# Performance work log

Hardware: AMD Instinct MI355X
Metric: run time of the kernel (lower is better)

Reference implementation:

```python
import jax, jax.numpy as jnp
import numpy as np

N = 16384      # total atoms (8 proteins x ~2048)
E = 524288     # N * max_neighbors(32)
B = 8          # graphs
F_IN = 26      # 20 residue types + 6 atom types
D = 128        # node_dim
H = 256        # hidden_dim
OUT = 64       # output_dim
L = 4          # n_layers
N_RBF = 16
CUTOFF = 10.0


def setup_inputs() -> dict:
    key = jax.random.key(0)
    ks = jax.random.split(key, 24)
    s = 0.05
    inp = {
        "positions": jax.random.normal(ks[0], (N, 3), jnp.float32) * 10.0,
        "node_features": jax.random.normal(ks[1], (N, F_IN), jnp.float32),
        "edge_index": jax.random.randint(ks[2], (2, E), 0, N, jnp.int32),
        "batch": jnp.sort(jax.random.randint(ks[3], (N,), 0, B, jnp.int32)),
        # node embedding MLP
        "emb_W1": jax.random.normal(ks[4], (F_IN, D), jnp.float32) * s,
        "emb_b1": jnp.zeros((D,), jnp.float32),
        "emb_W2": jax.random.normal(ks[5], (D, D), jnp.float32) * s,
        "emb_b2": jnp.zeros((D,), jnp.float32),
        # per-layer message MLP: [2D + n_rbf] -> H -> D
        "msg_W1": jax.random.normal(ks[6], (L, 2 * D + N_RBF, H), jnp.float32) * s,
        "msg_b1": jnp.zeros((L, H), jnp.float32),
        "msg_W2": jax.random.normal(ks[7], (L, H, D), jnp.float32) * s,
        "msg_b2": jnp.zeros((L, D), jnp.float32),
        # per-layer update MLP: [2D] -> H -> D (residual)
        "upd_W1": jax.random.normal(ks[8], (L, 2 * D, H), jnp.float32) * s,
        "upd_b1": jnp.zeros((L, H), jnp.float32),
        "upd_W2": jax.random.normal(ks[9], (L, H, D), jnp.float32) * s,
        "upd_b2": jnp.zeros((L, D), jnp.float32),
        # readout MLP: D -> H -> OUT
        "r_W1": jax.random.normal(ks[10], (D, H), jnp.float32) * s,
        "r_b1": jnp.zeros((H,), jnp.float32),
        "r_W2": jax.random.normal(ks[11], (H, OUT), jnp.float32) * s,
        "r_b2": jnp.zeros((OUT,), jnp.float32),
    }
    return inp


def _mlp2(x, W1, b1, W2, b2):
    return jax.nn.silu(x @ W1 + b1) @ W2 + b2


def _edge_rbf(positions, src, dst):
    rel = positions[dst] - positions[src]                      # (E,3)
    d = jnp.sqrt(jnp.sum(rel * rel, axis=-1) + 1e-12)          # (E,)
    centers = jnp.linspace(0.0, CUTOFF, N_RBF, dtype=positions.dtype)
    width = CUTOFF / N_RBF
    rbf = jnp.exp(-((d[:, None] - centers) ** 2) / (2.0 * width * width))  # (E,n_rbf)
    env = 0.5 * (jnp.cos(jnp.pi * d / CUTOFF) + 1.0) * (d < CUTOFF)        # cosine cutoff
    return rbf * env[:, None]


def reference(positions, node_features, edge_index, batch,
              emb_W1, emb_b1, emb_W2, emb_b2,
              msg_W1, msg_b1, msg_W2, msg_b2,
              upd_W1, upd_b1, upd_W2, upd_b2,
              r_W1, r_b1, r_W2, r_b2):
    src, dst = edge_index[0], edge_index[1]
    h = _mlp2(node_features, emb_W1, emb_b1, emb_W2, emb_b2)   # (N,D)
    ef = _edge_rbf(positions, src, dst)                        # (E,n_rbf)
    for i in range(L):
        m_in = jnp.concatenate([h[src], h[dst], ef], axis=-1)  # (E,2D+n_rbf)
        m = _mlp2(m_in, msg_W1[i], msg_b1[i], msg_W2[i], msg_b2[i])  # (E,D)
        agg = jax.ops.segment_sum(m, dst, num_segments=N)      # (N,D)
        u_in = jnp.concatenate([h, agg], axis=-1)              # (N,2D)
        h = h + _mlp2(u_in, upd_W1[i], upd_b1[i], upd_W2[i], upd_b2[i])
    # mean readout per graph
    counts = jax.ops.segment_sum(jnp.ones((N,), h.dtype), batch, num_segments=B)
    g = jax.ops.segment_sum(h, batch, num_segments=B) / jnp.maximum(counts, 1.0)[:, None]
    return _mlp2(g, r_W1, r_b1, r_W2, r_b2)                    # (B,OUT)
```

## Files before the change

### kernel.cpp

```cpp
#include <hip/hip_runtime.h>
#include <math.h>

#define NATOMS 16384
#define NEDGES 524288
#define NLAYERS 4
#define TE 64

typedef __bf16 bf16x8 __attribute__((ext_vector_type(8)));
typedef __bf16 bf16x4 __attribute__((ext_vector_type(4)));
typedef __bf16 bf16x2 __attribute__((ext_vector_type(2)));
typedef float f32x4 __attribute__((ext_vector_type(4)));

__device__ __forceinline__ float silu_f(float x) {
  return x * __builtin_amdgcn_rcpf(1.0f + __expf(-x));
}

__global__ __launch_bounds__(256) void hist_kernel(
    const int* __restrict__ dst, int* __restrict__ counts)
{
  int e = blockIdx.x * 256 + threadIdx.x;
  atomicAdd(&counts[dst[e]], 1);
}

__global__ __launch_bounds__(1024) void scan_kernel(
    const int* __restrict__ counts, int* __restrict__ cursor,
    float* __restrict__ degf)
{
  __shared__ int s_tot[1024];
  int tid = threadIdx.x;
  int v[16];
  {
    const int4* cp = (const int4*)(counts + tid * 16);
    int4 a = cp[0], b = cp[1], c = cp[2], d = cp[3];
    v[0]=a.x; v[1]=a.y; v[2]=a.z; v[3]=a.w;
    v[4]=b.x; v[5]=b.y; v[6]=b.z; v[7]=b.w;
    v[8]=c.x; v[9]=c.y; v[10]=c.z; v[11]=c.w;
    v[12]=d.x; v[13]=d.y; v[14]=d.z; v[15]=d.w;
  }
  int tot = 0;
  #pragma unroll
  for (int i = 0; i < 16; i++) tot += v[i];
  s_tot[tid] = tot;
  __syncthreads();
  for (int off = 1; off < 1024; off <<= 1) {
    int t = (tid >= off) ? s_tot[tid - off] : 0;
    __syncthreads();
    s_tot[tid] += t;
    __syncthreads();
  }
  int run = s_tot[tid] - tot;
  #pragma unroll
  for (int i = 0; i < 16; i++) {
    cursor[tid * 16 + i] = run;
    degf[tid * 16 + i] = (float)v[i];
    run += v[i];
  }
}

__global__ __launch_bounds__(256) void scatter_kernel(
    const int* __restrict__ src, const int* __restrict__ dst,
    int* __restrict__ cursor, int* __restrict__ esrc, int* __restrict__ edst)
{
  int e = blockIdx.x * 256 + threadIdx.x;
  int d = dst[e];
  int p = atomicAdd(&cursor[d], 1);
  esrc[p] = src[e];
  edst[p] = d;
}

__global__ __launch_bounds__(256) void prep_kernel(
    const float* __restrict__ mW1, const float* __restrict__ mW2,
    const float* __restrict__ uW1, const float* __restrict__ uW2,
    const float* __restrict__ mb2,
    __bf16* __restrict__ W1at, __bf16* __restrict__ W1bt,
    __bf16* __restrict__ B2c, __bf16* __restrict__ uW1ft,
    __bf16* __restrict__ uW2t, float* __restrict__ b2u)
{
  long l = blockIdx.y;
  int bx = blockIdx.x, tid = threadIdx.x;
  if (bx < 128) {
    int i = bx * 256 + tid;
    int n = i >> 7, k = i & 127;
    W1at[l * (256L * 128) + i] = (__bf16)mW1[l * (272L * 256) + (size_t)k * 256 + n];
  } else if (bx < 256) {
    int i = (bx - 128) * 256 + tid;
    int n = i >> 7, k = i & 127;
    W1bt[l * (256L * 128) + i] = (__bf16)mW1[l * (272L * 256) + (size_t)(128 + k) * 256 + n];
  } else if (bx < 288) {
    int i = (bx - 256) * 256 + tid;
    int c = i >> 5, k = i & 31;
    float v = (k < 16) ? mW1[l * (272L * 256) + (size_t)(256 + k) * 256 + c] : 0.0f;
    B2c[l * (256L * 32) + i] = (__bf16)v;
  } else if (bx < 672) {
    int i = (bx - 288) * 256 + tid;
    int n = i / 384, k = i - n * 384;
    float v;
    if (k < 128) {
      v = uW1[l * 65536 + (size_t)k * 256 + n];
    } else {
      int r = k - 128;
      v = 0.0f;
      for (int j = 0; j < 128; j++)
        v += mW2[(l * 256 + r) * 128 + j] * uW1[l * 65536 + (size_t)(128 + j) * 256 + n];
    }
    uW1ft[l * (256L * 384) + i] = (__bf16)v;
  } else if (bx < 800) {
    int i = (bx - 672) * 256 + tid;
    int n = i >> 8, k = i & 255;
    uW2t[l * (128L * 256) + i] = (__bf16)uW2[l * (256L * 128) + (size_t)k * 128 + n];
  } else {
    int c = tid;
    float acc = 0.0f;
    for (int j = 0; j < 128; j++)
      acc += mb2[l * 128 + j] * uW1[l * 65536 + (size_t)(128 + j) * 256 + c];
    b2u[l * 256 + c] = acc;
  }
}

__global__ __launch_bounds__(128) void embed_kernel(
    const float* __restrict__ x, const float* __restrict__ W1,
    const float* __restrict__ b1, const float* __restrict__ W2,
    const float* __restrict__ b2, float* __restrict__ h,
    __bf16* __restrict__ hb)
{
  int n = blockIdx.x;
  int j = threadIdx.x;
  __shared__ float xs[26];
  __shared__ float hid[128];
  if (j < 26) xs[j] = x[n * 26 + j];
  __syncthreads();
  float acc = b1[j];
  #pragma unroll
  for (int k = 0; k < 26; k++) acc += xs[k] * W1[k * 128 + j];
  hid[j] = silu_f(acc);
  __syncthreads();
  float acc2 = b2[j];
  #pragma unroll 8
  for (int k = 0; k < 128; k++) acc2 += hid[k] * W2[k * 128 + j];
  h[(size_t)n * 128 + j] = acc2;
  hb[(size_t)n * 128 + j] = (__bf16)acc2;
}

__global__ __launch_bounds__(256) void rbf_kernel(
    const float* __restrict__ pos, const int* __restrict__ esrc,
    const int* __restrict__ edst, __bf16* __restrict__ efb)
{
  int e = blockIdx.x * 256 + threadIdx.x;
  int s = esrc[e], d = edst[e];
  float dx = pos[d * 3 + 0] - pos[s * 3 + 0];
  float dy = pos[d * 3 + 1] - pos[s * 3 + 1];
  float dz = pos[d * 3 + 2] - pos[s * 3 + 2];
  float dist = sqrtf(dx * dx + dy * dy + dz * dz + 1e-12f);
  float env = (dist < 10.0f)
                  ? 0.5f * (cosf(3.14159265358979f * dist * 0.1f) + 1.0f)
                  : 0.0f;
  bf16x8 o0, o1;
  #pragma unroll
  for (int i = 0; i < 16; i++) {
    float c = (10.0f / 15.0f) * (float)i;
    float t = dist - c;
    float v = env * __expf(-t * t * 1.28f);
    if (i < 8) o0[i] = (__bf16)v; else o1[i - 8] = (__bf16)v;
  }
  *(bf16x8*)(efb + (size_t)e * 16 + 0) = o0;
  *(bf16x8*)(efb + (size_t)e * 16 + 8) = o1;
}

__global__ __launch_bounds__(256) void zprep_kernel(
    const __bf16* __restrict__ hb, const float* __restrict__ b1,
    const __bf16* __restrict__ W1at, const __bf16* __restrict__ W1bt,
    __bf16* __restrict__ z1b, __bf16* __restrict__ z2b, float* __restrict__ aggH)
{
  __shared__ __bf16 s_n[64][136];
  int tid = threadIdx.x, n0 = blockIdx.x * 64;
  {
    int n = tid >> 2, t4 = tid & 3;
    const bf16x8* hr = (const bf16x8*)(hb + (size_t)(n0 + n) * 128);
    #pragma unroll
    for (int i = 0; i < 4; i++)
      *(bf16x8*)&s_n[n][t4 * 8 + 32 * i] = hr[t4 + 4 * i];
  }
  {
    float4 zz = make_float4(0.f, 0.f, 0.f, 0.f);
    float4* ap = (float4*)(aggH + (size_t)n0 * 256);
    for (int i = tid; i < 64 * 256 / 4; i += 256) ap[i] = zz;
  }
  __syncthreads();
  const int wv = tid >> 6, ln = tid & 63, lc = ln & 15, qd = ln >> 4;
  for (int cp = 0; cp < 2; cp++) {
    f32x4 aA[4][2], aB[4][2];
    #pragma unroll
    for (int nt = 0; nt < 2; nt++) {
      float bv = b1[cp * 128 + wv * 32 + nt * 16 + lc];
      #pragma unroll
      for (int mt = 0; mt < 4; mt++) {
        aA[mt][nt][0] = 0.f; aA[mt][nt][1] = 0.f;
        aA[mt][nt][2] = 0.f; aA[mt][nt][3] = 0.f;
        aB[mt][nt][0] = bv; aB[mt][nt][1] = bv;
        aB[mt][nt][2] = bv; aB[mt][nt][3] = bv;
      }
    }
    #pragma unroll
    for (int kt = 0; kt < 4; kt++) {
      bf16x8 af[4];
      #pragma unroll
      for (int mt = 0; mt < 4; mt++)
        af[mt] = *(const bf16x8*)&s_n[mt * 16 + lc][kt * 32 + qd * 8];
      bf16x8 bwA[2], bwB[2];
      #pragma unroll
      for (int nt = 0; nt < 2; nt++) {
        int c = cp * 128 + wv * 32 + nt * 16 + lc;
        bwA[nt] = *(const bf16x8*)(W1at + (size_t)c * 128 + kt * 32 + qd * 8);
        bwB[nt] = *(const bf16x8*)(W1bt + (size_t)c * 128 + kt * 32 + qd * 8);
      }
      #pragma unroll
      for (int mt = 0; mt < 4; mt++)
        #pragma unroll
        for (int nt = 0; nt < 2; nt++) {
          aA[mt][nt] = __builtin_amdgcn_mfma_f32_16x16x32_bf16(af[mt], bwA[nt], aA[mt][nt], 0, 0, 0);
          aB[mt][nt] = __builtin_amdgcn_mfma_f32_16x16x32_bf16(af[mt], bwB[nt], aB[mt][nt], 0, 0, 0);
        }
    }
    #pragma unroll
    for (int mt = 0; mt < 4; mt++)
      #pragma unroll
      for (int nt = 0; nt < 2; nt++) {
        int c = cp * 128 + wv * 32 + nt * 16 + lc;
        #pragma unroll
        for (int r = 0; r < 4; r++) {
          int n = n0 + mt * 16 + qd * 4 + r;
          z1b[(size_t)n * 256 + c] = (__bf16)aA[mt][nt][r];
          z2b[(size_t)n * 256 + c] = (__bf16)aB[mt][nt][r];
        }
      }
  }
}

#define MS_EF_OFF   33792
#define MS_SRC_OFF  36864
#define MS_DST_OFF  37120
#define MS_MASK_OFF 37376
#define MS_BYTES    37392

__global__ __launch_bounds__(256, 4) void msg_mfma_kernel(
    const __bf16* __restrict__ z1b, const __bf16* __restrict__ z2b,
    const __bf16* __restrict__ efb,
    const int* __restrict__ esrc, const int* __restrict__ edst,
    const __bf16* __restrict__ B2c, float* __restrict__ aggH)
{
  __shared__ __align__(16) char smem[MS_BYTES];
  __bf16 (*s_hT)[66] = (__bf16(*)[66])(smem);
  __bf16 (*s_ef)[24] = (__bf16(*)[24])(smem + MS_EF_OFF);
  int* s_src = (int*)(smem + MS_SRC_OFF);
  int* s_dst = (int*)(smem + MS_DST_OFF);
  unsigned int* s_mask = (unsigned int*)(smem + MS_MASK_OFF);

  int tid = threadIdx.x, e0 = blockIdx.x * TE;

  if (tid < TE) {
    int d = edst[e0 + tid];
    s_dst[tid] = d;
    int dp = (tid == 0) ? (d ^ 1) : edst[e0 + tid - 1];
    unsigned long long mb = __ballot(d != dp);
    if (tid == 0) { s_mask[0] = (unsigned int)mb; s_mask[1] = (unsigned int)(mb >> 32); }
  } else if (tid < 2 * TE) {
    s_src[tid - TE] = esrc[e0 + tid - TE];
  }
  {
    int e = tid >> 2, t4 = tid & 3;
    if (t4 < 2)
      *(bf16x8*)&s_ef[e][t4 * 8] =
          *(const bf16x8*)(efb + (size_t)(e0 + e) * 16 + t4 * 8);
  }
  __syncthreads();

  const int wv = tid >> 6, ln = tid & 63, lc = ln & 15, qd = ln >> 4;

  bf16x8 bI;
  #pragma unroll
  for (int j = 0; j < 8; j++)
    bI[j] = (__bf16)((lc == (qd & 1) * 8 + j) ? 1.0f : 0.0f);

  const __bf16* pz[4];
  #pragma unroll
  for (int mt = 0; mt < 4; mt++) {
    int m = mt * 16 + lc;
    int row = (qd < 2) ? s_src[m] : s_dst[m];
    pz[mt] = ((qd < 2) ? z1b : z2b) + (size_t)row * 256 + (qd & 1) * 8;
  }

  #pragma unroll
  for (int hf = 0; hf < 2; hf++) {
    const int cb = hf * 128 + wv * 32;
    bf16x8 bw[2];
    #pragma unroll
    for (int nt = 0; nt < 2; nt++)
      bw[nt] = *(const bf16x8*)(B2c + (size_t)(cb + nt * 16 + lc) * 32 + qd * 8);

    #pragma unroll
    for (int mt = 0; mt < 4; mt++) {
      bf16x8 aef = *(const bf16x8*)&s_ef[mt * 16 + lc][(qd & 1) * 8];
      #pragma unroll
      for (int nt = 0; nt < 2; nt++) {
        bf16x8 az = *(const bf16x8*)(pz[mt] + cb + nt * 16);
        f32x4 z; z[0] = 0.f; z[1] = 0.f; z[2] = 0.f; z[3] = 0.f;
        f32x4 acc = __builtin_amdgcn_mfma_f32_16x16x32_bf16(az, bI, z, 0, 0, 0);
        acc = __builtin_amdgcn_mfma_f32_16x16x32_bf16(aef, bw[nt], acc, 0, 0, 0);
        bf16x2 p0, p1;
        p0[0] = (__bf16)silu_f(acc[0]); p0[1] = (__bf16)silu_f(acc[1]);
        p1[0] = (__bf16)silu_f(acc[2]); p1[1] = (__bf16)silu_f(acc[3]);
        __bf16* wp = &s_hT[cb + nt * 16 + lc][mt * 16 + qd * 4];
        *(bf16x2*)wp = p0;
        *(bf16x2*)(wp + 2) = p1;
      }
    }
  }
  __syncthreads();

  {
    const unsigned int mlo = __builtin_amdgcn_readfirstlane(s_mask[0]);
    const unsigned int mhi = __builtin_amdgcn_readfirstlane(s_mask[1]);
    int j = tid;
    float acc = 0.0f;
    int cur = s_dst[0];
    #pragma unroll 8
    for (int i = 0; i < 64; i += 2) {
      bf16x2 p = *(const bf16x2*)&s_hT[j][i];
      bool b0 = (i < 32) ? ((mlo >> i) & 1u) : ((mhi >> (i - 32)) & 1u);
      int i1 = i + 1;
      bool b1 = (i1 < 32) ? ((mlo >> i1) & 1u) : ((mhi >> (i1 - 32)) & 1u);
      if (i > 0 && b0) {
        atomicAdd(&aggH[(size_t)cur * 256 + j], acc);
        acc = 0.0f; cur = s_dst[i];
      }
      acc += (float)p[0];
      if (b1) {
        atomicAdd(&aggH[(size_t)cur * 256 + j], acc);
        acc = 0.0f; cur = s_dst[i1];
      }
      acc += (float)p[1];
    }
    atomicAdd(&aggH[(size_t)cur * 256 + j], acc);
  }
}

__global__ __launch_bounds__(512, 2) void upd_mfma_kernel(
    float* __restrict__ h, __bf16* __restrict__ hb,
    float* __restrict__ aggH, const float* __restrict__ degf,
    const __bf16* __restrict__ uW1ft, const float* __restrict__ b1,
    const float* __restrict__ b2u,
    const __bf16* __restrict__ uW2t, const float* __restrict__ b2,
    int do_z, const float* __restrict__ nb1,
    const __bf16* __restrict__ nW1at, const __bf16* __restrict__ nW1bt,
    __bf16* __restrict__ z1b, __bf16* __restrict__ z2b)
{
  __shared__ __bf16 s_u[64][392];
  __shared__ __bf16 s_uh[64][264];
  int tid = threadIdx.x, n0 = blockIdx.x * 64;
  {
    int n = tid >> 3, t8 = tid & 7;
    const bf16x8* hr = (const bf16x8*)(hb + (size_t)(n0 + n) * 128);
    #pragma unroll
    for (int i = 0; i < 2; i++)
      *(bf16x8*)&s_u[n][t8 * 8 + 64 * i] = hr[t8 + 8 * i];
    const float* sr = aggH + (size_t)(n0 + n) * 256;
    #pragma unroll
    for (int i = 0; i < 4; i++) {
      int col = t8 * 8 + i * 64;
      float4 a = *(const float4*)(sr + col);
      float4 b = *(const float4*)(sr + col + 4);
      bf16x8 o;
      o[0] = (__bf16)a.x; o[1] = (__bf16)a.y; o[2] = (__bf16)a.z; o[3] = (__bf16)a.w;
      o[4] = (__bf16)b.x; o[5] = (__bf16)b.y; o[6] = (__bf16)b.z; o[7] = (__bf16)b.w;
      *(bf16x8*)&s_u[n][128 + col] = o;
    }
  }
  __syncthreads();
  const int wv = tid >> 6, ln = tid & 63, lc = ln & 15, qd = ln >> 4;

  float dg[4][4];
  #pragma unroll
  for (int mt = 0; mt < 4; mt++)
    #pragma unroll
    for (int r = 0; r < 4; r++)
      dg[mt][r] = degf[n0 + mt * 16 + qd * 4 + r];

  {
    f32x4 acc1[4][2];
    #pragma unroll
    for (int nt = 0; nt < 2; nt++) {
      int c = wv * 32 + nt * 16 + lc;
      float bv = b1[c];
      float b2uv = b2u[c];
      #pragma unroll
      for (int mt = 0; mt < 4; mt++)
        #pragma unroll
        for (int r = 0; r < 4; r++)
          acc1[mt][nt][r] = bv + dg[mt][r] * b2uv;
    }
    #pragma unroll
    for (int kt = 0; kt < 12; kt++) {
      bf16x8 af[4];
      #pragma unroll
      for (int mt = 0; mt < 4; mt++)
        af[mt] = *(const bf16x8*)&s_u[mt * 16 + lc][kt * 32 + qd * 8];
      bf16x8 bw[2];
      #pragma unroll
      for (int nt = 0; nt < 2; nt++)
        bw[nt] = *(const bf16x8*)(uW1ft +
                 (size_t)(wv * 32 + nt * 16 + lc) * 384 + kt * 32 + qd * 8);
      #pragma unroll
      for (int mt = 0; mt < 4; mt++)
        #pragma unroll
        for (int nt = 0; nt < 2; nt++)
          acc1[mt][nt] = __builtin_amdgcn_mfma_f32_16x16x32_bf16(af[mt], bw[nt], acc1[mt][nt], 0, 0, 0);
    }
    #pragma unroll
    for (int mt = 0; mt < 4; mt++)
      #pragma unroll
      for (int nt = 0; nt < 2; nt++) {
        int cc = wv * 32 + nt * 16 + lc;
        #pragma unroll
        for (int r = 0; r < 4; r++)
          s_uh[mt * 16 + qd * 4 + r][cc] = (__bf16)silu_f(acc1[mt][nt][r]);
      }
  }
  __syncthreads();

  const int ow = wv * 16 + lc;
  f32x4 acc2[4];
  {
    float bv = b2[ow];
    #pragma unroll
    for (int mt = 0; mt < 4; mt++) {
      acc2[mt][0] = bv; acc2[mt][1] = bv; acc2[mt][2] = bv; acc2[mt][3] = bv;
    }
  }
  #pragma unroll
  for (int kt = 0; kt < 8; kt++) {
    bf16x8 a2[4];
    #pragma unroll
    for (int mt = 0; mt < 4; mt++)
      a2[mt] = *(const bf16x8*)&s_uh[mt * 16 + lc][kt * 32 + qd * 8];
    bf16x8 b2w = *(const bf16x8*)(uW2t + (size_t)ow * 256 + kt * 32 + qd * 8);
    #pragma unroll
    for (int mt = 0; mt < 4; mt++)
      acc2[mt] = __builtin_amdgcn_mfma_f32_16x16x32_bf16(a2[mt], b2w, acc2[mt], 0, 0, 0);
  }

  #pragma unroll
  for (int mt = 0; mt < 4; mt++)
    #pragma unroll
    for (int r = 0; r < 4; r++) {
      int n = n0 + mt * 16 + qd * 4 + r;
      float v = h[(size_t)n * 128 + ow] + acc2[mt][r];
      h[(size_t)n * 128 + ow] = v;
      hb[(size_t)n * 128 + ow] = (__bf16)v;
    }

  if (do_z) {
    __syncthreads();
    {
      float4 zz = make_float4(0.f, 0.f, 0.f, 0.f);
      float4* ap = (float4*)(aggH + (size_t)n0 * 256);
      for (int i = tid; i < 64 * 256 / 4; i += 512) ap[i] = zz;
      int n = tid >> 3, t8 = tid & 7;
      const bf16x8* hr = (const bf16x8*)(hb + (size_t)(n0 + n) * 128);
      #pragma unroll
      for (int i = 0; i < 2; i++)
        *(bf16x8*)&s_u[n][t8 * 8 + 64 * i] = hr[t8 + 8 * i];
    }
    __syncthreads();
    f32x4 aA[4][2], aB[4][2];
    #pragma unroll
    for (int nt = 0; nt < 2; nt++) {
      float bv = nb1[wv * 32 + nt * 16 + lc];
      #pragma unroll
      for (int mt = 0; mt < 4; mt++) {
        aA[mt][nt][0] = 0.f; aA[mt][nt][1] = 0.f;
        aA[mt][nt][2] = 0.f; aA[mt][nt][3] = 0.f;
        aB[mt][nt][0] = bv; aB[mt][nt][1] = bv;
        aB[mt][nt][2] = bv; aB[mt][nt][3] = bv;
      }
    }
    #pragma unroll
    for (int kt = 0; kt < 4; kt++) {
      bf16x8 af[4];
      #pragma unroll
      for (int mt = 0; mt < 4; mt++)
        af[mt] = *(const bf16x8*)&s_u[mt * 16 + lc][kt * 32 + qd * 8];
      bf16x8 bwA[2], bwB[2];
      #pragma unroll
      for (int nt = 0; nt < 2; nt++) {
        int c = wv * 32 + nt * 16 + lc;
        bwA[nt] = *(const bf16x8*)(nW1at + (size_t)c * 128 + kt * 32 + qd * 8);
        bwB[nt] = *(const bf16x8*)(nW1bt + (size_t)c * 128 + kt * 32 + qd * 8);
      }
      #pragma unroll
      for (int mt = 0; mt < 4; mt++)
        #pragma unroll
        for (int nt = 0; nt < 2; nt++) {
          aA[mt][nt] = __builtin_amdgcn_mfma_f32_16x16x32_bf16(af[mt], bwA[nt], aA[mt][nt], 0, 0, 0);
          aB[mt][nt] = __builtin_amdgcn_mfma_f32_16x16x32_bf16(af[mt], bwB[nt], aB[mt][nt], 0, 0, 0);
        }
    }
    #pragma unroll
    for (int mt = 0; mt < 4; mt++)
      #pragma unroll
      for (int nt = 0; nt < 2; nt++) {
        int c = wv * 32 + nt * 16 + lc;
        #pragma unroll
        for (int r = 0; r < 4; r++) {
          int n = n0 + mt * 16 + qd * 4 + r;
          z1b[(size_t)n * 256 + c] = (__bf16)aA[mt][nt][r];
          z2b[(size_t)n * 256 + c] = (__bf16)aB[mt][nt][r];
        }
      }
  }
}

__global__ __launch_bounds__(128) void readout_sum_kernel(
    const float* __restrict__ h, const int* __restrict__ batch,
    float* __restrict__ gsum, float* __restrict__ gcnt)
{
  int j = threadIdx.x;
  int n0 = blockIdx.x * 128;
  float acc = 0.f, cacc = 0.f;
  int cur = batch[n0];
  for (int i = 0; i < 128; i++) {
    int b = batch[n0 + i];
    if (b != cur) {
      atomicAdd(&gsum[cur * 128 + j], acc);
      if (j == 0) atomicAdd(&gcnt[cur], cacc);
      acc = 0.f; cacc = 0.f; cur = b;
    }
    acc += h[(size_t)(n0 + i) * 128 + j];
    cacc += 1.f;
  }
  atomicAdd(&gsum[cur * 128 + j], acc);
  if (j == 0) atomicAdd(&gcnt[cur], cacc);
}

__global__ __launch_bounds__(256) void readout_mlp_kernel(
    const float* __restrict__ gsum, const float* __restrict__ gcnt,
    const float* __restrict__ W1, const float* __restrict__ b1,
    const float* __restrict__ W2, const float* __restrict__ b2,
    float* __restrict__ out)
{
  __shared__ float g[8][128];
  __shared__ float hid[8][256];
  int tid = threadIdx.x;
  for (int i = tid; i < 8 * 128; i += 256) {
    int b = i >> 7, c = i & 127;
    g[b][c] = gsum[i] / fmaxf(gcnt[b], 1.0f);
  }
  __syncthreads();
  {
    float bb = b1[tid];
    float a[8];
    #pragma unroll
    for (int b = 0; b < 8; b++) a[b] = bb;
    for (int k = 0; k < 128; k++) {
      float w = W1[k * 256 + tid];
      #pragma unroll
      for (int b = 0; b < 8; b++) a[b] += g[b][k] * w;
    }
    #pragma unroll
    for (int b = 0; b < 8; b++) hid[b][tid] = silu_f(a[b]);
  }
  __syncthreads();
  int j = tid & 63, bg = tid >> 6;
  float a0 = b2[j], a1 = b2[j];
  for (int k = 0; k < 256; k++) {
    float w = W2[k * 64 + j];
    a0 += hid[bg * 2 + 0][k] * w;
    a1 += hid[bg * 2 + 1][k] * w;
  }
  out[(bg * 2 + 0) * 64 + j] = a0;
  out[(bg * 2 + 1) * 64 + j] = a1;
}

extern "C" void kernel_launch(void* const* d_in, const int* in_sizes, int n_in,
                              void* d_out, int out_size, void* d_ws, size_t ws_size,
                              hipStream_t stream) {
  const float* pos   = (const float*)d_in[0];
  const float* xfeat = (const float*)d_in[1];
  const int*   eidx  = (const int*)d_in[2];
  const int*   batch = (const int*)d_in[3];
  const float* eW1 = (const float*)d_in[4];
  const float* eb1 = (const float*)d_in[5];
  const float* eW2 = (const float*)d_in[6];
  const float* eb2 = (const float*)d_in[7];
  const float* mW1 = (const float*)d_in[8];
  const float* mb1 = (const float*)d_in[9];
  const float* mW2 = (const float*)d_in[10];
  const float* mb2 = (const float*)d_in[11];
  const float* uW1 = (const float*)d_in[12];
  const float* ub1 = (const float*)d_in[13];
  const float* uW2 = (const float*)d_in[14];
  const float* ub2 = (const float*)d_in[15];
  const float* rW1 = (const float*)d_in[16];
  const float* rb1 = (const float*)d_in[17];
  const float* rW2 = (const float*)d_in[18];
  const float* rb2 = (const float*)d_in[19];

  const int* srcI = eidx;
  const int* dstI = eidx + NEDGES;

  char* base = (char*)d_ws;
  float* h    = (float*)base;  base += (size_t)NATOMS * 128 * 4;
  float* aggH = (float*)base;  base += (size_t)NATOMS * 256 * 4;
  __bf16* z1b = (__bf16*)base; base += (size_t)NATOMS * 256 * 2;
  __bf16* z2b = (__bf16*)base; base += (size_t)NATOMS * 256 * 2;
  __bf16* hb  = (__bf16*)base; base += (size_t)NATOMS * 128 * 2;
  __bf16* efb = (__bf16*)base; base += (size_t)NEDGES * 16 * 2;
  __bf16* W1at = (__bf16*)base; base += (size_t)NLAYERS * 256 * 128 * 2;
  __bf16* W1bt = (__bf16*)base; base += (size_t)NLAYERS * 256 * 128 * 2;
  __bf16* B2c  = (__bf16*)base; base += (size_t)NLAYERS * 256 * 32 * 2;
  __bf16* uW1ft = (__bf16*)base; base += (size_t)NLAYERS * 256 * 384 * 2;
  __bf16* uW2t = (__bf16*)base; base += (size_t)NLAYERS * 128 * 256 * 2;
  float* b2u  = (float*)base;  base += (size_t)NLAYERS * 256 * 4;
  float* degf = (float*)base;  base += (size_t)NATOMS * 4;
  float* gsum = (float*)base;  base += 8 * 128 * 4;
  float* gcnt = (float*)base;  base += 8 * 4;
  int* counts = (int*)base;    base += (size_t)NATOMS * 4;
  int* cursor = (int*)base;    base += (size_t)NATOMS * 4;
  int* esrc   = (int*)base;    base += (size_t)NEDGES * 4;
  int* edst   = (int*)base;    base += (size_t)NEDGES * 4;

  hipMemsetAsync(counts, 0, NATOMS * sizeof(int), stream);
  hist_kernel<<<NEDGES / 256, 256, 0, stream>>>(dstI, counts);
  scan_kernel<<<1, 1024, 0, stream>>>(counts, cursor, degf);
  scatter_kernel<<<NEDGES / 256, 256, 0, stream>>>(srcI, dstI, cursor, esrc, edst);

  prep_kernel<<<dim3(801, NLAYERS), 256, 0, stream>>>(
      mW1, mW2, uW1, uW2, mb2, W1at, W1bt, B2c, uW1ft, uW2t, b2u);

  embed_kernel<<<NATOMS, 128, 0, stream>>>(xfeat, eW1, eb1, eW2, eb2, h, hb);
  rbf_kernel<<<NEDGES / 256, 256, 0, stream>>>(pos, esrc, edst, efb);

  zprep_kernel<<<NATOMS / 64, 256, 0, stream>>>(
      hb, mb1, W1at, W1bt, z1b, z2b, aggH);

  for (int l = 0; l < NLAYERS; l++) {
    int ln = (l < NLAYERS - 1) ? (l + 1) : l;
    msg_mfma_kernel<<<NEDGES / TE, 256, 0, stream>>>(
        z1b, z2b, efb, esrc, edst,
        B2c + (size_t)l * 256 * 32, aggH);
    upd_mfma_kernel<<<NATOMS / 64, 512, 0, stream>>>(
        h, hb, aggH, degf,
        uW1ft + (size_t)l * 256 * 384, ub1 + (size_t)l * 256,
        b2u + (size_t)l * 256,
        uW2t + (size_t)l * 128 * 256, ub2 + (size_t)l * 128,
        (l < NLAYERS - 1) ? 1 : 0,
        mb1 + (size_t)ln * 256,
        W1at + (size_t)ln * 256 * 128, W1bt + (size_t)ln * 256 * 128,
        z1b, z2b);
  }

  hipMemsetAsync(gsum, 0, (8 * 128 + 8) * sizeof(float), stream);
  readout_sum_kernel<<<NATOMS / 128, 128, 0, stream>>>(h, batch, gsum, gcnt);
  readout_mlp_kernel<<<1, 256, 0, stream>>>(gsum, gcnt, rW1, rb1, rW2, rb2,
                                            (float*)d_out);
}
```

Measured before the change: 674.9 us.

## Fuse embedding MLP into zprep and enlarge message edge tile to 128

The node embedding MLP is folded into the zprep kernel, so h is computed per 64-node tile and fed straight into shared memory, which removes one launch and a global round trip of hb. The message kernel now handles 128 edges per block with 512 threads: each wave covers one 32-column slice across 8 row tiles, and the segmented-sum reduction is split into two 64-edge halves with per-wave ballot masks. This halves the number of message blocks and gives more reuse per block, at the cost of doubling shared memory and lowering occupancy to 2 blocks per CU. The embedding now uses 32 scalar accumulators per thread with strided weight reads, which may be slower than the old per-node kernel.

```diff
diff --git a/kernel.cpp b/kernel.cpp
--- a/kernel.cpp
+++ b/kernel.cpp
@@ -4,7 +4,7 @@
 #define NATOMS 16384
 #define NEDGES 524288
 #define NLAYERS 4
-#define TE 64
+#define TE 128
 
 typedef __bf16 bf16x8 __attribute__((ext_vector_type(8)));
 typedef __bf16 bf16x4 __attribute__((ext_vector_type(4)));
@@ -117,30 +117,6 @@
   }
 }
 
-__global__ __launch_bounds__(128) void embed_kernel(
-    const float* __restrict__ x, const float* __restrict__ W1,
-    const float* __restrict__ b1, const float* __restrict__ W2,
-    const float* __restrict__ b2, float* __restrict__ h,
-    __bf16* __restrict__ hb)
-{
-  int n = blockIdx.x;
-  int j = threadIdx.x;
-  __shared__ float xs[26];
-  __shared__ float hid[128];
-  if (j < 26) xs[j] = x[n * 26 + j];
-  __syncthreads();
-  float acc = b1[j];
-  #pragma unroll
-  for (int k = 0; k < 26; k++) acc += xs[k] * W1[k * 128 + j];
-  hid[j] = silu_f(acc);
-  __syncthreads();
-  float acc2 = b2[j];
-  #pragma unroll 8
-  for (int k = 0; k < 128; k++) acc2 += hid[k] * W2[k * 128 + j];
-  h[(size_t)n * 128 + j] = acc2;
-  hb[(size_t)n * 128 + j] = (__bf16)acc2;
-}
-
 __global__ __launch_bounds__(256) void rbf_kernel(
     const float* __restrict__ pos, const int* __restrict__ esrc,
     const int* __restrict__ edst, __bf16* __restrict__ efb)
@@ -166,19 +142,22 @@
   *(bf16x8*)(efb + (size_t)e * 16 + 8) = o1;
 }
 
-__global__ __launch_bounds__(256) void zprep_kernel(
-    const __bf16* __restrict__ hb, const float* __restrict__ b1,
+__global__ __launch_bounds__(256) void embed_zprep_kernel(
+    const float* __restrict__ x, const float* __restrict__ eW1,
+    const float* __restrict__ eb1, const float* __restrict__ eW2,
+    const float* __restrict__ eb2, const float* __restrict__ b1,
     const __bf16* __restrict__ W1at, const __bf16* __restrict__ W1bt,
-    __bf16* __restrict__ z1b, __bf16* __restrict__ z2b, float* __restrict__ aggH)
-{
+    float* __restrict__ h, __bf16* __restrict__ hb,
+    __bf16* __restrict__ z1b, __bf16* __restrict__ z2b,
+    float* __restrict__ aggH)
+{
+  __shared__ float s_x[64][28];
+  __shared__ float s_hid[64][132];
   __shared__ __bf16 s_n[64][136];
   int tid = threadIdx.x, n0 = blockIdx.x * 64;
-  {
-    int n = tid >> 2, t4 = tid & 3;
-    const bf16x8* hr = (const bf16x8*)(hb + (size_t)(n0 + n) * 128);
-    #pragma unroll
-    for (int i = 0; i < 4; i++)
-      *(bf16x8*)&s_n[n][t4 * 8 + 32 * i] = hr[t4 + 4 * i];
+  for (int i = tid; i < 64 * 26; i += 256) {
+    int n = i / 26, c = i - n * 26;
+    s_x[n][c] = x[(size_t)(n0 + n) * 26 + c];
   }
   {
     float4 zz = make_float4(0.f, 0.f, 0.f, 0.f);
@@ -186,6 +165,38 @@
     for (int i = tid; i < 64 * 256 / 4; i += 256) ap[i] = zz;
   }
   __syncthreads();
+  {
+    int n = tid >> 2, j0 = (tid & 3) * 32;
+    float acc[32];
+    #pragma unroll
+    for (int jj = 0; jj < 32; jj++) acc[jj] = eb1[j0 + jj];
+    for (int k = 0; k < 26; k++) {
+      float xv = s_x[n][k];
+      #pragma unroll
+      for (int jj = 0; jj < 32; jj++)
+        acc[jj] += xv * eW1[k * 128 + j0 + jj];
+    }
+    #pragma unroll
+    for (int jj = 0; jj < 32; jj++) s_hid[n][j0 + jj] = silu_f(acc[jj]);
+    __syncthreads();
+    #pragma unroll
+    for (int jj = 0; jj < 32; jj++) acc[jj] = eb2[j0 + jj];
+    for (int k = 0; k < 128; k++) {
+      float hv = s_hid[n][k];
+      #pragma unroll
+      for (int jj = 0; jj < 32; jj++)
+        acc[jj] += hv * eW2[k * 128 + j0 + jj];
+    }
+    #pragma unroll
+    for (int jj = 0; jj < 32; jj++) {
+      float v = acc[jj];
+      h[(size_t)(n0 + n) * 128 + j0 + jj] = v;
+      hb[(size_t)(n0 + n) * 128 + j0 + jj] = (__bf16)v;
+      s_n[n][j0 + jj] = (__bf16)v;
+    }
+  }
+  __syncthreads();
+
   const int wv = tid >> 6, ln = tid & 63, lc = ln & 15, qd = ln >> 4;
   for (int cp = 0; cp < 2; cp++) {
     f32x4 aA[4][2], aB[4][2];
@@ -236,20 +247,20 @@
   }
 }
 
-#define MS_EF_OFF   33792
-#define MS_SRC_OFF  36864
-#define MS_DST_OFF  37120
-#define MS_MASK_OFF 37376
-#define MS_BYTES    37392
-
-__global__ __launch_bounds__(256, 4) void msg_mfma_kernel(
+#define MS_EF_OFF   66560
+#define MS_SRC_OFF  72704
+#define MS_DST_OFF  73216
+#define MS_MASK_OFF 73728
+#define MS_BYTES    73744
+
+__global__ __launch_bounds__(512, 2) void msg_mfma_kernel(
     const __bf16* __restrict__ z1b, const __bf16* __restrict__ z2b,
     const __bf16* __restrict__ efb,
     const int* __restrict__ esrc, const int* __restrict__ edst,
     const __bf16* __restrict__ B2c, float* __restrict__ aggH)
 {
   __shared__ __align__(16) char smem[MS_BYTES];
-  __bf16 (*s_hT)[66] = (__bf16(*)[66])(smem);
+  __bf16 (*s_hT)[130] = (__bf16(*)[130])(smem);
   __bf16 (*s_ef)[24] = (__bf16(*)[24])(smem + MS_EF_OFF);
   int* s_src = (int*)(smem + MS_SRC_OFF);
   int* s_dst = (int*)(smem + MS_DST_OFF);
@@ -262,7 +273,11 @@
     s_dst[tid] = d;
     int dp = (tid == 0) ? (d ^ 1) : edst[e0 + tid - 1];
     unsigned long long mb = __ballot(d != dp);
-    if (tid == 0) { s_mask[0] = (unsigned int)mb; s_mask[1] = (unsigned int)(mb >> 32); }
+    if ((tid & 63) == 0) {
+      int w = (tid >> 6) * 2;
+      s_mask[w] = (unsigned int)mb;
+      s_mask[w + 1] = (unsigned int)(mb >> 32);
+    }
   } else if (tid < 2 * TE) {
     s_src[tid - TE] = esrc[e0 + tid - TE];
   }
@@ -281,66 +296,63 @@
   for (int j = 0; j < 8; j++)
     bI[j] = (__bf16)((lc == (qd & 1) * 8 + j) ? 1.0f : 0.0f);
 
-  const __bf16* pz[4];
-  #pragma unroll
-  for (int mt = 0; mt < 4; mt++) {
+  const __bf16* pz[8];
+  #pragma unroll
+  for (int mt = 0; mt < 8; mt++) {
     int m = mt * 16 + lc;
     int row = (qd < 2) ? s_src[m] : s_dst[m];
     pz[mt] = ((qd < 2) ? z1b : z2b) + (size_t)row * 256 + (qd & 1) * 8;
   }
 
-  #pragma unroll
-  for (int hf = 0; hf < 2; hf++) {
-    const int cb = hf * 128 + wv * 32;
-    bf16x8 bw[2];
-    #pragma unroll
-    for (int nt = 0; nt < 2; nt++)
-      bw[nt] = *(const bf16x8*)(B2c + (size_t)(cb + nt * 16 + lc) * 32 + qd * 8);
-
-    #pragma unroll
-    for (int mt = 0; mt < 4; mt++) {
-      bf16x8 aef = *(const bf16x8*)&s_ef[mt * 16 + lc][(qd & 1) * 8];
-      #pragma unroll
-      for (int nt = 0; nt < 2; nt++) {
-        bf16x8 az = *(const bf16x8*)(pz[mt] + cb + nt * 16);
-        f32x4 z; z[0] = 0.f; z[1] = 0.f; z[2] = 0.f; z[3] = 0.f;
-        f32x4 acc = __builtin_amdgcn_mfma_f32_16x16x32_bf16(az, bI, z, 0, 0, 0);
-        acc = __builtin_amdgcn_mfma_f32_16x16x32_bf16(aef, bw[nt], acc, 0, 0, 0);
-        bf16x2 p0, p1;
-        p0[0] = (__bf16)silu_f(acc[0]); p0[1] = (__bf16)silu_f(acc[1]);
-        p1[0] = (__bf16)silu_f(acc[2]); p1[1] = (__bf16)silu_f(acc[3]);
-        __bf16* wp = &s_hT[cb + nt * 16 + lc][mt * 16 + qd * 4];
-        *(bf16x2*)wp = p0;
-        *(bf16x2*)(wp + 2) = p1;
-      }
-    }
-  }
-  __syncthreads();
-
-  {
-    const unsigned int mlo = __builtin_amdgcn_readfirstlane(s_mask[0]);
-    const unsigned int mhi = __builtin_amdgcn_readfirstlane(s_mask[1]);
-    int j = tid;
+  const int cb = wv * 32;
+  bf16x8 bw[2];
+  #pragma unroll
+  for (int nt = 0; nt < 2; nt++)
+    bw[nt] = *(const bf16x8*)(B2c + (size_t)(cb + nt * 16 + lc) * 32 + qd * 8);
+
+  #pragma unroll
+  for (int mt = 0; mt < 8; mt++) {
+    bf16x8 aef = *(const bf16x8*)&s_ef[mt * 16 + lc][(qd & 1) * 8];
+    #pragma unroll
+    for (int nt = 0; nt < 2; nt++) {
+      bf16x8 az = *(const bf16x8*)(pz[mt] + cb + nt * 16);
+      f32x4 z; z[0] = 0.f; z[1] = 0.f; z[2] = 0.f; z[3] = 0.f;
+      f32x4 acc = __builtin_amdgcn_mfma_f32_16x16x32_bf16(az, bI, z, 0, 0, 0);
+      acc = __builtin_amdgcn_mfma_f32_16x16x32_bf16(aef, bw[nt], acc, 0, 0, 0);
+      bf16x2 p0, p1;
+      p0[0] = (__bf16)silu_f(acc[0]); p0[1] = (__bf16)silu_f(acc[1]);
+      p1[0] = (__bf16)silu_f(acc[2]); p1[1] = (__bf16)silu_f(acc[3]);
+      __bf16* wp = &s_hT[cb + nt * 16 + lc][mt * 16 + qd * 4];
+      *(bf16x2*)wp = p0;
+      *(bf16x2*)(wp + 2) = p1;
+    }
+  }
+  __syncthreads();
+
+  {
+    int col = tid & 255, half = tid >> 8, r0 = half * 64;
+    const unsigned int mlo = __builtin_amdgcn_readfirstlane(s_mask[half * 2]);
+    const unsigned int mhi = __builtin_amdgcn_readfirstlane(s_mask[half * 2 + 1]);
     float acc = 0.0f;
-    int cur = s_dst[0];
+    int cur = s_dst[r0];
     #pragma unroll 8
     for (int i = 0; i < 64; i += 2) {
-      bf16x2 p = *(const bf16x2*)&s_hT[j][i];
+      bf16x2 p = *(const bf16x2*)&s_hT[col][r0 + i];
       bool b0 = (i < 32) ? ((mlo >> i) & 1u) : ((mhi >> (i - 32)) & 1u);
       int i1 = i + 1;
       bool b1 = (i1 < 32) ? ((mlo >> i1) & 1u) : ((mhi >> (i1 - 32)) & 1u);
       if (i > 0 && b0) {
-        atomicAdd(&aggH[(size_t)cur * 256 + j], acc);
-        acc = 0.0f; cur = s_dst[i];
+        atomicAdd(&aggH[(size_t)cur * 256 + col], acc);
+        acc = 0.0f; cur = s_dst[r0 + i];
       }
       acc += (float)p[0];
       if (b1) {
-        atomicAdd(&aggH[(size_t)cur * 256 + j], acc);
-        acc = 0.0f; cur = s_dst[i1];
+        atomicAdd(&aggH[(size_t)cur * 256 + col], acc);
+        acc = 0.0f; cur = s_dst[r0 + i1];
       }
       acc += (float)p[1];
     }
-    atomicAdd(&aggH[(size_t)cur * 256 + j], acc);
+    atomicAdd(&aggH[(size_t)cur * 256 + col], acc);
   }
 }
 
@@ -636,15 +648,14 @@
   prep_kernel<<<dim3(801, NLAYERS), 256, 0, stream>>>(
       mW1, mW2, uW1, uW2, mb2, W1at, W1bt, B2c, uW1ft, uW2t, b2u);
 
-  embed_kernel<<<NATOMS, 128, 0, stream>>>(xfeat, eW1, eb1, eW2, eb2, h, hb);
   rbf_kernel<<<NEDGES / 256, 256, 0, stream>>>(pos, esrc, edst, efb);
 
-  zprep_kernel<<<NATOMS / 64, 256, 0, stream>>>(
-      hb, mb1, W1at, W1bt, z1b, z2b, aggH);
+  embed_zprep_kernel<<<NATOMS / 64, 256, 0, stream>>>(
+      xfeat, eW1, eb1, eW2, eb2, mb1, W1at, W1bt, h, hb, z1b, z2b, aggH);
 
   for (int l = 0; l < NLAYERS; l++) {
     int ln = (l < NLAYERS - 1) ? (l + 1) : l;
-    msg_mfma_kernel<<<NEDGES / TE, 256, 0, stream>>>(
+    msg_mfma_kernel<<<NEDGES / TE, 512, 0, stream>>>(
         z1b, z2b, efb, esrc, edst,
         B2c + (size_t)l * 256 * 32, aggH);
     upd_mfma_kernel<<<NATOMS / 64, 512, 0, stream>>>(
```

After: 793.3 us. 17.6% more time.
